# Optimization experiments

Hardware: AMD Instinct MI355X
Metric: run time of the kernel (lower is better)

## Reference

```python
import jax, jax.numpy as jnp
import numpy as np

B = 64        # graphs per batch
N_PER = 1024  # nodes per graph
DEG = 16      # avg degree
H = 128       # hidden width


def _graph_conv(x, src, dst, emask, Wr, b, Wl):
    # PyG GraphConv: out_i = W_rel @ sum_{j->i} x_j + b + W_root @ x_i
    msg = x[src] * emask[:, None]                       # [E, F]
    agg = jax.ops.segment_sum(msg, dst, num_segments=x.shape[0])
    return agg @ Wr + x @ Wl + b


def _topk_pool(x, w, nmask, src, dst, emask, ratio=0.8):
    # PyG TopKPooling: score = (x @ w)/||w||, keep top ceil(ratio*n_i) per graph,
    # kept x scaled by tanh(score). Expressed with masks (fixed shapes).
    score = (x @ w) / jnp.linalg.norm(w)                # [N]
    score = jnp.where(nmask > 0, score, -jnp.inf)
    s2 = score.reshape(B, -1)
    rank = jnp.argsort(jnp.argsort(-s2, axis=1), axis=1)  # rank 0 = largest score
    counts = nmask.reshape(B, -1).sum(axis=1)
    k = jnp.ceil(ratio * counts)
    keep = (rank < k[:, None]).reshape(-1).astype(x.dtype)
    x_new = x * jnp.where(keep > 0, jnp.tanh(score), 0.0)[:, None]
    emask_new = emask * keep[src] * keep[dst]
    return x_new, keep, emask_new


def _readout(x, nmask):
    # concat(global_max_pool, global_mean_pool) over surviving nodes per graph
    xg = x.reshape(B, -1, x.shape[-1])
    m = nmask.reshape(B, -1, 1)
    mx = jnp.max(jnp.where(m > 0, xg, -jnp.inf), axis=1)
    mn = (xg * m).sum(axis=1) / m.sum(axis=1)
    return jnp.concatenate([mx, mn], axis=1)            # [B, 2H]


def setup_inputs():
    key = jax.random.key(0)
    ks = jax.random.split(key, 16)
    N = B * N_PER
    x = jax.random.normal(ks[0], (N, 4), dtype=jnp.float32)
    e_per = N_PER * DEG
    off = (jnp.arange(B) * N_PER)[:, None]
    src = (jax.random.randint(ks[1], (B, e_per), 0, N_PER) + off).reshape(-1)
    dst = (jax.random.randint(ks[2], (B, e_per), 0, N_PER) + off).reshape(-1)
    edge_index = jnp.stack([src, dst]).astype(jnp.int32)

    def lin(k, fi, fo, s=0.1):
        return jax.random.normal(k, (fi, fo), dtype=jnp.float32) * s

    return {
        "x": x, "edge_index": edge_index,
        "w1r": lin(ks[3], 4, H), "b1": jnp.zeros((H,), jnp.float32), "w1l": lin(ks[4], 4, H),
        "w2r": lin(ks[5], H, H), "b2": jnp.zeros((H,), jnp.float32), "w2l": lin(ks[6], H, H),
        "w3r": lin(ks[7], H, H), "b3": jnp.zeros((H,), jnp.float32), "w3l": lin(ks[8], H, H),
        "p1w": jax.random.normal(ks[9], (H,), jnp.float32) * 0.1,
        "p2w": jax.random.normal(ks[10], (H,), jnp.float32) * 0.1,
        "w_lin1": lin(ks[11], 2 * H, H), "b_lin1": jnp.zeros((H,), jnp.float32),
        "w_lin2": lin(ks[12], H, 64), "b_lin2": jnp.zeros((64,), jnp.float32),
        "w_lin3": lin(ks[13], 64, 7), "b_lin3": jnp.zeros((7,), jnp.float32),
    }


def reference(x, edge_index, w1r, b1, w1l, w2r, b2, w2l, w3r, b3, w3l,
              p1w, p2w, w_lin1, b_lin1, w_lin2, b_lin2, w_lin3, b_lin3):
    src, dst = edge_index[0], edge_index[1]
    nmask = jnp.ones((x.shape[0],), x.dtype)
    emask = jnp.ones((src.shape[0],), x.dtype)

    h = jax.nn.relu(_graph_conv(x, src, dst, emask, w1r, b1, w1l)) * nmask[:, None]
    h, nmask, emask = _topk_pool(h, p1w, nmask, src, dst, emask)
    x1 = _readout(h, nmask)

    h = jax.nn.relu(_graph_conv(h, src, dst, emask, w2r, b2, w2l)) * nmask[:, None]
    h, nmask, emask = _topk_pool(h, p2w, nmask, src, dst, emask)
    x2 = _readout(h, nmask)

    h = jax.nn.relu(_graph_conv(h, src, dst, emask, w3r, b3, w3l)) * nmask[:, None]
    # NOTE: original forward reuses self.pool2 for the third pooling (pool3 unused)
    h, nmask, emask = _topk_pool(h, p2w, nmask, src, dst, emask)
    x3 = _readout(h, nmask)

    z = x1 + x2 + x3
    z = jax.nn.relu(z @ w_lin1 + b_lin1)
    # F.dropout with training=False (eval) is identity
    z = jax.nn.relu(z @ w_lin2 + b_lin2)
    return jax.nn.log_softmax(z @ w_lin3 + b_lin3, axis=-1)  # [B, 7]
```

## Files before the change

### kernel.cpp

```cpp
#include <hip/hip_runtime.h>
#include <hip/hip_bf16.h>
#include <math.h>

#define NN   65536
#define NG   64
#define NPER 1024
#define NE   1048576
#define EPG  16384
#define HD   128
#define K1 820
#define K2 656
#define K3 525

typedef unsigned short u16;
typedef unsigned int   u32;
typedef __attribute__((ext_vector_type(8))) short short8;
typedef __attribute__((ext_vector_type(4))) float floatx4;

__device__ __forceinline__ float bf2f(u16 u) {
    union { u32 i; float f; } v; v.i = ((u32)u) << 16; return v.f;
}
__device__ __forceinline__ u16 f2bf(float f) {
    u32 x = __float_as_uint(f);
    return (u16)((x + 0x7fffu + ((x >> 16) & 1u)) >> 16);
}
__device__ __forceinline__ float ldx(const void* p, size_t i, int bf) {
    return bf ? bf2f(((const u16*)p)[i]) : ((const float*)p)[i];
}

__global__ void k_sentinel(u32* out) {
    if (threadIdx.x < 224) out[threadIdx.x] = 0x46404640u;
}

__global__ __launch_bounds__(1024) void k_csr(const int* __restrict__ src,
                                              const int* __restrict__ dst,
                                              int* __restrict__ row_ptr,
                                              int* __restrict__ col,
                                              const void* __restrict__ x,
                                              int* __restrict__ flag) {
    __shared__ int s_scan[1024];
    __shared__ int s_cur[1024];
    int g = blockIdx.x, t = threadIdx.x;
    if (g == 64) {
        int ok = 0;
        if (t < 256) {
            u16 u = ((const u16*)x)[2 * t];
            int e = (u >> 7) & 0xFF;
            ok = (e >= 100 && e <= 140) ? 1 : 0;
        }
        s_scan[t] = ok;
        __syncthreads();
        for (int off = 512; off; off >>= 1) {
            if (t < off) s_scan[t] += s_scan[t + off];
            __syncthreads();
        }
        if (t == 0) flag[0] = (s_scan[0] >= 192) ? 1 : 0;
        return;
    }
    int ebase = g * EPG;
    s_scan[t] = 0;
    __syncthreads();
    #pragma unroll
    for (int i = 0; i < 16; i++) {
        int dd = dst[ebase + i * 1024 + t] - g * NPER;
        atomicAdd(&s_scan[dd], 1);
    }
    __syncthreads();
    int v = s_scan[t];
    __syncthreads();
    s_scan[t] = v;
    __syncthreads();
    for (int off = 1; off < 1024; off <<= 1) {
        int x2 = (t >= off) ? s_scan[t - off] : 0;
        __syncthreads();
        s_scan[t] += x2;
        __syncthreads();
    }
    int excl = s_scan[t] - v;
    row_ptr[g * NPER + t] = ebase + excl;
    if (g == 0 && t == 0) row_ptr[NN] = NE;
    s_cur[t] = excl;
    __syncthreads();
    #pragma unroll
    for (int i = 0; i < 16; i++) {
        int e = ebase + i * 1024 + t;
        int dd = dst[e] - g * NPER;
        int p = atomicAdd(&s_cur[dd], 1);
        col[ebase + p] = src[e];
    }
}

__global__ void k_pack_w(const void* __restrict__ W2r, const void* __restrict__ W2l,
                         const void* __restrict__ W3r, const void* __restrict__ W3l,
                         u16* __restrict__ hi2, u16* __restrict__ lo2,
                         u16* __restrict__ hi3, u16* __restrict__ lo3,
                         const int* __restrict__ flag) {
    const int bf = *flag;
    int which = blockIdx.x >> 7;
    const void* Wr = which ? W3r : W2r;
    const void* Wl = which ? W3l : W2l;
    u16* hi = which ? hi3 : hi2;
    u16* lo = which ? lo3 : lo2;
    int idx = (blockIdx.x & 127) * 256 + threadIdx.x;
    int j = idx & 7;
    int lane = (idx >> 3) & 63;
    int c = (idx >> 9) & 7;
    int t = idx >> 12;
    int k = c * 32 + ((lane >> 4) << 3) + j;
    int n = t * 16 + (lane & 15);
    float w = (k < HD) ? ldx(Wr, (size_t)k * HD + n, bf)
                       : ldx(Wl, (size_t)(k - HD) * HD + n, bf);
    u16 h = f2bf(w);
    hi[idx] = h;
    lo[idx] = f2bf(w - bf2f(h));
}

__global__ void k_conv1(const void* __restrict__ x, const int* __restrict__ row_ptr,
                        const int* __restrict__ col,
                        const void* __restrict__ w1r, const void* __restrict__ b1,
                        const void* __restrict__ w1l, float* __restrict__ hout,
                        const void* __restrict__ pw, float* __restrict__ score,
                        const int* __restrict__ flag) {
    const int bf = *flag;
    int wave = threadIdx.x >> 6, lane = threadIdx.x & 63;
    int node = (blockIdx.x & 63) * NPER + (blockIdx.x >> 6) * 4 + wave;
    int rp = row_ptr[node], rq = row_ptr[node + 1];
    float a0 = 0.f, a1 = 0.f, a2 = 0.f, a3 = 0.f;
    for (int j = rp + lane; j < rq; j += 64) {
        int s = col[j];
        if (bf) {
            ushort4 u = *(const ushort4*)((const u16*)x + (size_t)s * 4);
            a0 += bf2f(u.x); a1 += bf2f(u.y); a2 += bf2f(u.z); a3 += bf2f(u.w);
        } else {
            float4 u = *(const float4*)((const float*)x + (size_t)s * 4);
            a0 += u.x; a1 += u.y; a2 += u.z; a3 += u.w;
        }
    }
    for (int m = 32; m; m >>= 1) {
        a0 += __shfl_xor(a0, m, 64);
        a1 += __shfl_xor(a1, m, 64);
        a2 += __shfl_xor(a2, m, 64);
        a3 += __shfl_xor(a3, m, 64);
    }
    float x0, x1, x2, x3;
    if (bf) {
        ushort4 u = *(const ushort4*)((const u16*)x + (size_t)node * 4);
        x0 = bf2f(u.x); x1 = bf2f(u.y); x2 = bf2f(u.z); x3 = bf2f(u.w);
    } else {
        float4 u = *(const float4*)((const float*)x + (size_t)node * 4);
        x0 = u.x; x1 = u.y; x2 = u.z; x3 = u.w;
    }
    float vout[2];
    #pragma unroll
    for (int rep = 0; rep < 2; rep++) {
        int o = lane + rep * 64;
        float v = ldx(b1, o, bf);
        v += a0 * ldx(w1r, 0 * HD + o, bf) + a1 * ldx(w1r, 1 * HD + o, bf)
           + a2 * ldx(w1r, 2 * HD + o, bf) + a3 * ldx(w1r, 3 * HD + o, bf);
        v += x0 * ldx(w1l, 0 * HD + o, bf) + x1 * ldx(w1l, 1 * HD + o, bf)
           + x2 * ldx(w1l, 2 * HD + o, bf) + x3 * ldx(w1l, 3 * HD + o, bf);
        v = fmaxf(v, 0.f);
        vout[rep] = v;
        hout[(size_t)node * HD + o] = v;
    }
    float w0 = ldx(pw, lane, bf), w1 = ldx(pw, lane + 64, bf);
    float dot = vout[0] * w0 + vout[1] * w1;
    float nrm = w0 * w0 + w1 * w1;
    for (int m = 32; m; m >>= 1) {
        dot += __shfl_xor(dot, m, 64);
        nrm += __shfl_xor(nrm, m, 64);
    }
    if (lane == 0) score[node] = dot / sqrtf(nrm);
}

__global__ __launch_bounds__(256) void k_pool2(
    const float* __restrict__ score, const float* __restrict__ prev_keep,
    float* __restrict__ out_keep, float* __restrict__ out_val,
    const float* __restrict__ h, float* __restrict__ pmax, float* __restrict__ psum,
    int K) {
    __shared__ __align__(16) float s_sc[1024];
    __shared__ int s_r[256];
    __shared__ float s_val[128], s_keep[128];
    __shared__ float s_mx[8][128], s_sm[8][128];
    int g = blockIdx.x & 63, chunk = blockIdx.x >> 6;
    int t = threadIdx.x;
    #pragma unroll
    for (int i = 0; i < 4; i++) {
        int j = t + i * 256;
        float sc = score[g * NPER + j];
        if (prev_keep && prev_keep[g * NPER + j] == 0.f) sc = -INFINITY;
        s_sc[j] = sc;
    }
    __syncthreads();
    int nloc = chunk * 128 + (t & 127);
    int half = t >> 7;
    float sc = s_sc[nloc];
    int r = 0;
    #pragma unroll 4
    for (int j4 = half * 128; j4 < half * 128 + 128; j4++) {
        float4 sv = *(const float4*)&s_sc[j4 * 4];
        int j = j4 * 4;
        r += (int)((sv.x > sc) || (sv.x == sc && j     < nloc));
        r += (int)((sv.y > sc) || (sv.y == sc && j + 1 < nloc));
        r += (int)((sv.z > sc) || (sv.z == sc && j + 2 < nloc));
        r += (int)((sv.w > sc) || (sv.w == sc && j + 3 < nloc));
    }
    s_r[t] = r;
    __syncthreads();
    if (t < 128) {
        int rt = s_r[t] + s_r[t + 128];
        bool kp = rt < K;
        float kpf = kp ? 1.f : 0.f;
        float vv = kp ? tanhf(sc) : 0.f;
        out_keep[g * NPER + nloc] = kpf;
        out_val[g * NPER + nloc] = vv;
        s_keep[t] = kpf;
        s_val[t] = vv;
    }
    __syncthreads();
    int cg = t & 31, slot = t >> 5;
    float4 mx = {-INFINITY, -INFINITY, -INFINITY, -INFINITY};
    float4 sm = {0.f, 0.f, 0.f, 0.f};
    #pragma unroll 4
    for (int i = 0; i < 16; i++) {
        int nn = slot * 16 + i;
        float vv = s_val[nn], kp = s_keep[nn];
        const float* hp = h + (size_t)(g * NPER + chunk * 128 + nn) * HD + cg * 4;
        float4 v = *(const float4*)hp;
        v.x *= vv; v.y *= vv; v.z *= vv; v.w *= vv;
        sm.x += v.x; sm.y += v.y; sm.z += v.z; sm.w += v.w;
        if (kp != 0.f) {
            mx.x = fmaxf(mx.x, v.x); mx.y = fmaxf(mx.y, v.y);
            mx.z = fmaxf(mx.z, v.z); mx.w = fmaxf(mx.w, v.w);
        }
    }
    *(float4*)&s_mx[slot][cg * 4] = mx;
    *(float4*)&s_sm[slot][cg * 4] = sm;
    __syncthreads();
    if (t < 128) {
        float M = s_mx[0][t], S = s_sm[0][t];
        #pragma unroll
        for (int s = 1; s < 8; s++) {
            M = fmaxf(M, s_mx[s][t]);
            S += s_sm[s][t];
        }
        size_t o = (size_t)(chunk * 64 + g) * HD + t;
        pmax[o] = M;
        psum[o] = S;
    }
}

__global__ __launch_bounds__(256) void k_agg(const float* __restrict__ h,
                      const float* __restrict__ val,
                      const int* __restrict__ row_ptr,
                      const int* __restrict__ col, float* __restrict__ agg) {
    int g = blockIdx.x & 63, chunk = blockIdx.x >> 6;
    int wave = threadIdx.x >> 6, lane = threadIdx.x & 63;
    int node = g * NPER + chunk * 4 + wave;
    int rp = row_ptr[node], rq = row_ptr[node + 1];
    int deg = rq - rp;
    int e = lane >> 4, c = lane & 15;
    float4 acc0 = {0.f, 0.f, 0.f, 0.f}, acc1 = {0.f, 0.f, 0.f, 0.f};
    for (int base = 0; base < deg; base += 64) {
        int bcnt = min(64, deg - base);
        int myidx = col[rp + base + ((lane < bcnt) ? lane : 0)];
        int m = 0;
        for (; m + 8 <= bcnt; m += 8) {
            int s0 = __shfl(myidx, m + e, 64);
            int s1 = __shfl(myidx, m + 4 + e, 64);
            float vs0 = val[s0], vs1 = val[s1];
            const float* p0 = h + (size_t)s0 * HD + c * 4;
            const float* p1 = h + (size_t)s1 * HD + c * 4;
            float4 va = *(const float4*)p0;
            float4 vb = *(const float4*)(p0 + 64);
            float4 vc = *(const float4*)p1;
            float4 vd = *(const float4*)(p1 + 64);
            acc0.x += va.x * vs0; acc0.y += va.y * vs0; acc0.z += va.z * vs0; acc0.w += va.w * vs0;
            acc1.x += vb.x * vs0; acc1.y += vb.y * vs0; acc1.z += vb.z * vs0; acc1.w += vb.w * vs0;
            acc0.x += vc.x * vs1; acc0.y += vc.y * vs1; acc0.z += vc.z * vs1; acc0.w += vc.w * vs1;
            acc1.x += vd.x * vs1; acc1.y += vd.y * vs1; acc1.z += vd.z * vs1; acc1.w += vd.w * vs1;
        }
        if (m + 4 <= bcnt) {
            int s0 = __shfl(myidx, m + e, 64);
            float vs0 = val[s0];
            const float* p0 = h + (size_t)s0 * HD + c * 4;
            float4 va = *(const float4*)p0;
            float4 vb = *(const float4*)(p0 + 64);
            acc0.x += va.x * vs0; acc0.y += va.y * vs0; acc0.z += va.z * vs0; acc0.w += va.w * vs0;
            acc1.x += vb.x * vs0; acc1.y += vb.y * vs0; acc1.z += vb.z * vs0; acc1.w += vb.w * vs0;
            m += 4;
        }
        int rem = bcnt - m;
        if (rem > 0) {
            int s0 = __shfl(myidx, m + ((e < rem) ? e : 0), 64);
            float vs0 = val[s0];
            const float* p0 = h + (size_t)s0 * HD + c * 4;
            float4 va = *(const float4*)p0;
            float4 vb = *(const float4*)(p0 + 64);
            if (e < rem) {
                acc0.x += va.x * vs0; acc0.y += va.y * vs0; acc0.z += va.z * vs0; acc0.w += va.w * vs0;
                acc1.x += vb.x * vs0; acc1.y += vb.y * vs0; acc1.z += vb.z * vs0; acc1.w += vb.w * vs0;
            }
        }
    }
    acc0.x += __shfl_xor(acc0.x, 16, 64); acc0.x += __shfl_xor(acc0.x, 32, 64);
    acc0.y += __shfl_xor(acc0.y, 16, 64); acc0.y += __shfl_xor(acc0.y, 32, 64);
    acc0.z += __shfl_xor(acc0.z, 16, 64); acc0.z += __shfl_xor(acc0.z, 32, 64);
    acc0.w += __shfl_xor(acc0.w, 16, 64); acc0.w += __shfl_xor(acc0.w, 32, 64);
    acc1.x += __shfl_xor(acc1.x, 16, 64); acc1.x += __shfl_xor(acc1.x, 32, 64);
    acc1.y += __shfl_xor(acc1.y, 16, 64); acc1.y += __shfl_xor(acc1.y, 32, 64);
    acc1.z += __shfl_xor(acc1.z, 16, 64); acc1.z += __shfl_xor(acc1.z, 32, 64);
    acc1.w += __shfl_xor(acc1.w, 16, 64); acc1.w += __shfl_xor(acc1.w, 32, 64);
    if (e == 0) {
        *(float4*)(agg + (size_t)node * HD + c * 4) = acc0;
        *(float4*)(agg + (size_t)node * HD + 64 + c * 4) = acc1;
    }
}

__global__ __launch_bounds__(256) void k_gemm_mfma(
    const float* __restrict__ agg, const float* __restrict__ h,
    const u16* __restrict__ whi, const u16* __restrict__ wlo,
    const void* __restrict__ bias, const float* __restrict__ keep,
    const float* __restrict__ val, float* __restrict__ out,
    const void* __restrict__ pw, float* __restrict__ score,
    const int* __restrict__ flag) {
    const int bf = *flag;
    int t = threadIdx.x;
    int w = t >> 6, lane = t & 63;
    int quad = lane >> 4;
    int m0 = (blockIdx.x & 63) * NPER + (blockIdx.x >> 6) * 64 + w * 16;
    int mrow = m0 + (lane & 15);
    float vrow = val[mrow];

    floatx4 acc[8];
    #pragma unroll
    for (int i = 0; i < 8; i++) acc[i] = (floatx4)0.f;

    #pragma unroll
    for (int c = 0; c < 8; c++) {
        const float* src = (c < 4) ? agg : h;
        int kb = (c & 3) * 32 + quad * 8;
        const float* pa = src + (size_t)mrow * HD + kb;
        float4 a0 = *(const float4*)pa;
        float4 a1 = *(const float4*)(pa + 4);
        float av[8] = {a0.x, a0.y, a0.z, a0.w, a1.x, a1.y, a1.z, a1.w};
        short8 ahi, alo;
        #pragma unroll
        for (int j = 0; j < 8; j++) {
            float a = (c < 4) ? av[j] : av[j] * vrow;
            u16 hb = f2bf(a);
            ahi[j] = (short)hb;
            alo[j] = (short)f2bf(a - bf2f(hb));
        }
        #pragma unroll
        for (int tt = 0; tt < 8; tt++) {
            const u16* bp = whi + (((size_t)(tt * 8 + c) * 64 + lane) << 3);
            short8 bhi = *(const short8*)bp;
            acc[tt] = __builtin_amdgcn_mfma_f32_16x16x32_bf16(ahi, bhi, acc[tt], 0, 0, 0);
            acc[tt] = __builtin_amdgcn_mfma_f32_16x16x32_bf16(alo, bhi, acc[tt], 0, 0, 0);
        }
        if (!bf) {
            #pragma unroll
            for (int tt = 0; tt < 8; tt++) {
                const u16* bp = wlo + (((size_t)(tt * 8 + c) * 64 + lane) << 3);
                short8 blo = *(const short8*)bp;
                acc[tt] = __builtin_amdgcn_mfma_f32_16x16x32_bf16(ahi, blo, acc[tt], 0, 0, 0);
            }
        }
    }

    float kf[4];
    #pragma unroll
    for (int r = 0; r < 4; r++) kf[r] = keep[m0 + quad * 4 + r];
    float sp0 = 0.f, sp1 = 0.f, sp2 = 0.f, sp3 = 0.f, nrm = 0.f;
    #pragma unroll
    for (int tt = 0; tt < 8; tt++) {
        int colc = tt * 16 + (lane & 15);
        float bcol = ldx(bias, colc, bf);
        float wv = ldx(pw, colc, bf);
        nrm += wv * wv;
        #pragma unroll
        for (int r = 0; r < 4; r++) {
            int row = m0 + quad * 4 + r;
            float v = fmaxf(acc[tt][r] + bcol, 0.f) * kf[r];
            out[(size_t)row * HD + colc] = v;
            if (r == 0) sp0 += v * wv;
            else if (r == 1) sp1 += v * wv;
            else if (r == 2) sp2 += v * wv;
            else sp3 += v * wv;
        }
    }
    #pragma unroll
    for (int m = 1; m < 16; m <<= 1) {
        sp0 += __shfl_xor(sp0, m, 64);
        sp1 += __shfl_xor(sp1, m, 64);
        sp2 += __shfl_xor(sp2, m, 64);
        sp3 += __shfl_xor(sp3, m, 64);
        nrm += __shfl_xor(nrm, m, 64);
    }
    if ((lane & 15) == 0) {
        float inv = 1.f / sqrtf(nrm);
        float4 sc;
        sc.x = sp0 * inv; sc.y = sp1 * inv; sc.z = sp2 * inv; sc.w = sp3 * inv;
        *(float4*)(score + m0 + quad * 4) = sc;
    }
}

__global__ __launch_bounds__(256) void k_mlp(
    const float* __restrict__ pmax1, const float* __restrict__ psum1,
    const float* __restrict__ pmax2, const float* __restrict__ psum2,
    const float* __restrict__ pmax3, const float* __restrict__ psum3,
    const void* __restrict__ w1, const void* __restrict__ b1,
    const void* __restrict__ w2, const void* __restrict__ b2,
    const void* __restrict__ w3, const void* __restrict__ b3,
    void* __restrict__ out, const int* __restrict__ flag) {
    const int bf = *flag;
    int g = blockIdx.x, t = threadIdx.x;
    __shared__ float sIn[256], sZ1[128], sZ2[64], sZ3[7], sRed[2];
    __shared__ float sP1[2][128];
    __shared__ float sP2[4][64];
    if (t < 128) {
        float M1 = -INFINITY, M2 = -INFINITY, M3 = -INFINITY;
        #pragma unroll
        for (int ch = 0; ch < 8; ch++) {
            size_t o = (size_t)(ch * 64 + g) * HD + t;
            M1 = fmaxf(M1, pmax1[o]);
            M2 = fmaxf(M2, pmax2[o]);
            M3 = fmaxf(M3, pmax3[o]);
        }
        sIn[t] = M1 + M2 + M3;
    } else {
        int c = t - 128;
        float S1 = 0.f, S2 = 0.f, S3 = 0.f;
        #pragma unroll
        for (int ch = 0; ch < 8; ch++) {
            size_t o = (size_t)(ch * 64 + g) * HD + c;
            S1 += psum1[o];
            S2 += psum2[o];
            S3 += psum3[o];
        }
        sIn[t] = S1 / (float)K1 + S2 / (float)K2 + S3 / (float)K3;
    }
    __syncthreads();
    {
        int o = t & 127, half = t >> 7;
        float v = 0.f;
        #pragma unroll 8
        for (int k = half * 128; k < half * 128 + 128; k++)
            v += sIn[k] * ldx(w1, (size_t)k * 128 + o, bf);
        sP1[half][o] = v;
    }
    __syncthreads();
    if (t < 128) sZ1[t] = fmaxf(sP1[0][t] + sP1[1][t] + ldx(b1, t, bf), 0.f);
    __syncthreads();
    {
        int o = t & 63, seg = t >> 6;
        float v = 0.f;
        #pragma unroll 8
        for (int k = seg * 32; k < seg * 32 + 32; k++)
            v += sZ1[k] * ldx(w2, (size_t)k * 64 + o, bf);
        sP2[seg][o] = v;
    }
    __syncthreads();
    if (t < 64) sZ2[t] = fmaxf(sP2[0][t] + sP2[1][t] + sP2[2][t] + sP2[3][t]
                               + ldx(b2, t, bf), 0.f);
    __syncthreads();
    if (t < 7) {
        float v = ldx(b3, t, bf);
        #pragma unroll 8
        for (int k = 0; k < 64; k++) v += sZ2[k] * ldx(w3, (size_t)k * 7 + t, bf);
        sZ3[t] = v;
    }
    __syncthreads();
    if (t == 0) {
        float mx = sZ3[0];
        for (int i = 1; i < 7; i++) mx = fmaxf(mx, sZ3[i]);
        float s = 0.f;
        for (int i = 0; i < 7; i++) s += expf(sZ3[i] - mx);
        sRed[0] = mx; sRed[1] = logf(s);
    }
    __syncthreads();
    if (t < 7) {
        float v = sZ3[t] - sRed[0] - sRed[1];
        if (bf) {
            __hip_bfloat16 hb = __float2bfloat16(v);
            ((u16*)out)[g * 7 + t] = *(u16*)&hb;
        } else {
            ((float*)out)[g * 7 + t] = v;
        }
    }
}

extern "C" void kernel_launch(void* const* d_in, const int* in_sizes, int n_in,
                              void* d_out, int out_size, void* d_ws, size_t ws_size,
                              hipStream_t stream) {
    (void)in_sizes; (void)n_in; (void)out_size;
    const void* x   = d_in[0];
    const int* ei   = (const int*)d_in[1];
    const void* w1r = d_in[2];
    const void* b1  = d_in[3];
    const void* w1l = d_in[4];
    const void* w2r = d_in[5];
    const void* b2  = d_in[6];
    const void* w2l = d_in[7];
    const void* w3r = d_in[8];
    const void* b3  = d_in[9];
    const void* w3l = d_in[10];
    const void* p1w = d_in[11];
    const void* p2w = d_in[12];
    const void* wl1 = d_in[13];
    const void* bl1 = d_in[14];
    const void* wl2 = d_in[15];
    const void* bl2 = d_in[16];
    const void* wl3 = d_in[17];
    const void* bl3 = d_in[18];
    const int* srcI = ei;
    const int* dstI = ei + NE;

    char* base = (char*)d_ws;
    char* p = base;
    auto alloc = [&](size_t bytes) -> char* {
        char* r = p; p += (bytes + 255) & ~(size_t)255; return r;
    };
    float* bufA   = (float*)alloc((size_t)NN * HD * 4);
    float* bufB   = (float*)alloc((size_t)NN * HD * 4);
    int* row_ptr  = (int*)alloc((size_t)(NN + 1) * 4);
    int* colA     = (int*)alloc((size_t)NE * 4);
    float* keep1  = (float*)alloc((size_t)NN * 4);
    float* keep2  = (float*)alloc((size_t)NN * 4);
    float* keep3  = (float*)alloc((size_t)NN * 4);
    float* score  = (float*)alloc((size_t)NN * 4);
    float* val1   = (float*)alloc((size_t)NN * 4);
    float* val2   = (float*)alloc((size_t)NN * 4);
    float* val3   = (float*)alloc((size_t)NN * 4);
    float* pmax1  = (float*)alloc((size_t)8 * NG * HD * 4);
    float* psum1  = (float*)alloc((size_t)8 * NG * HD * 4);
    float* pmax2  = (float*)alloc((size_t)8 * NG * HD * 4);
    float* psum2  = (float*)alloc((size_t)8 * NG * HD * 4);
    float* pmax3  = (float*)alloc((size_t)8 * NG * HD * 4);
    float* psum3  = (float*)alloc((size_t)8 * NG * HD * 4);
    int* flag     = (int*)alloc(256);
    u16* whi2     = (u16*)alloc((size_t)32768 * 2);
    u16* wlo2     = (u16*)alloc((size_t)32768 * 2);
    u16* whi3     = (u16*)alloc((size_t)32768 * 2);
    u16* wlo3     = (u16*)alloc((size_t)32768 * 2);

    if ((size_t)(p - base) > ws_size) {
        k_sentinel<<<1, 256, 0, stream>>>((u32*)d_out);
        return;
    }

    k_csr<<<NG + 1, 1024, 0, stream>>>(srcI, dstI, row_ptr, colA, x, flag);
    k_pack_w<<<256, 256, 0, stream>>>(w2r, w2l, w3r, w3l, whi2, wlo2, whi3, wlo3, flag);

    k_conv1<<<NN / 4, 256, 0, stream>>>(x, row_ptr, colA, w1r, b1, w1l, bufA,
                                        p1w, score, flag);
    k_pool2<<<NG * 8, 256, 0, stream>>>(score, nullptr, keep1, val1, bufA,
                                        pmax1, psum1, K1);

    k_agg<<<NN / 4, 256, 0, stream>>>(bufA, val1, row_ptr, colA, bufB);
    k_gemm_mfma<<<NN / 64, 256, 0, stream>>>(bufB, bufA, whi2, wlo2, b2, keep1, val1,
                                             bufB, p2w, score, flag);
    k_pool2<<<NG * 8, 256, 0, stream>>>(score, keep1, keep2, val2, bufB,
                                        pmax2, psum2, K2);

    k_agg<<<NN / 4, 256, 0, stream>>>(bufB, val2, row_ptr, colA, bufA);
    k_gemm_mfma<<<NN / 64, 256, 0, stream>>>(bufA, bufB, whi3, wlo3, b3, keep2, val2,
                                             bufA, p2w, score, flag);
    k_pool2<<<NG * 8, 256, 0, stream>>>(score, keep2, keep3, val3, bufA,
                                        pmax3, psum3, K3);

    k_mlp<<<NG, 256, 0, stream>>>(pmax1, psum1, pmax2, psum2, pmax3, psum3,
                                  wl1, bl1, wl2, bl2, wl3, bl3, d_out, flag);
}
```

Before: 364.3 us.

## Fuse neighbor aggregation into MFMA GEMM and merge weight packing into CSR prep

Removes the separate aggregation kernel: each GEMM block stages its CSR column slice in LDS and each lane gathers and sums neighbor features directly into registers that feed the MFMA A operand. This drops the write and reread of a full aggregated feature buffer and one launch per layer. Weight packing is folded into the CSR build kernel as extra blocks that recompute the dtype flag locally, removing another launch. The tradeoff is less parallelism for the gather, with each lane walking edges serially, and higher register pressure.

```diff
diff --git a/kernel.cpp b/kernel.cpp
--- a/kernel.cpp
+++ b/kernel.cpp
@@ -32,16 +32,18 @@
     if (threadIdx.x < 224) out[threadIdx.x] = 0x46404640u;
 }
 
-__global__ __launch_bounds__(1024) void k_csr(const int* __restrict__ src,
-                                              const int* __restrict__ dst,
-                                              int* __restrict__ row_ptr,
-                                              int* __restrict__ col,
-                                              const void* __restrict__ x,
-                                              int* __restrict__ flag) {
+__global__ __launch_bounds__(1024) void k_prep(
+    const int* __restrict__ src, const int* __restrict__ dst,
+    int* __restrict__ row_ptr, int* __restrict__ col,
+    const void* __restrict__ x, int* __restrict__ flag,
+    const void* __restrict__ W2r, const void* __restrict__ W2l,
+    const void* __restrict__ W3r, const void* __restrict__ W3l,
+    u16* __restrict__ hi2, u16* __restrict__ lo2,
+    u16* __restrict__ hi3, u16* __restrict__ lo3) {
     __shared__ int s_scan[1024];
     __shared__ int s_cur[1024];
-    int g = blockIdx.x, t = threadIdx.x;
-    if (g == 64) {
+    int b = blockIdx.x, t = threadIdx.x;
+    if (b >= 64) {
         int ok = 0;
         if (t < 256) {
             u16 u = ((const u16*)x)[2 * t];
@@ -54,9 +56,32 @@
             if (t < off) s_scan[t] += s_scan[t + off];
             __syncthreads();
         }
-        if (t == 0) flag[0] = (s_scan[0] >= 192) ? 1 : 0;
+        int bf = (s_scan[0] >= 192) ? 1 : 0;
+        if (b == 64) {
+            if (t == 0) flag[0] = bf;
+            return;
+        }
+        int pb = b - 65;
+        int which = pb >> 5;
+        const void* Wr = which ? W3r : W2r;
+        const void* Wl = which ? W3l : W2l;
+        u16* hi = which ? hi3 : hi2;
+        u16* lo = which ? lo3 : lo2;
+        int idx = (pb & 31) * 1024 + t;
+        int j = idx & 7;
+        int lane = (idx >> 3) & 63;
+        int c = (idx >> 9) & 7;
+        int tt = idx >> 12;
+        int k = c * 32 + ((lane >> 4) << 3) + j;
+        int n = tt * 16 + (lane & 15);
+        float w = (k < HD) ? ldx(Wr, (size_t)k * HD + n, bf)
+                           : ldx(Wl, (size_t)(k - HD) * HD + n, bf);
+        u16 h = f2bf(w);
+        hi[idx] = h;
+        lo[idx] = f2bf(w - bf2f(h));
         return;
     }
+    int g = b;
     int ebase = g * EPG;
     s_scan[t] = 0;
     __syncthreads();
@@ -88,31 +113,6 @@
         int p = atomicAdd(&s_cur[dd], 1);
         col[ebase + p] = src[e];
     }
-}
-
-__global__ void k_pack_w(const void* __restrict__ W2r, const void* __restrict__ W2l,
-                         const void* __restrict__ W3r, const void* __restrict__ W3l,
-                         u16* __restrict__ hi2, u16* __restrict__ lo2,
-                         u16* __restrict__ hi3, u16* __restrict__ lo3,
-                         const int* __restrict__ flag) {
-    const int bf = *flag;
-    int which = blockIdx.x >> 7;
-    const void* Wr = which ? W3r : W2r;
-    const void* Wl = which ? W3l : W2l;
-    u16* hi = which ? hi3 : hi2;
-    u16* lo = which ? lo3 : lo2;
-    int idx = (blockIdx.x & 127) * 256 + threadIdx.x;
-    int j = idx & 7;
-    int lane = (idx >> 3) & 63;
-    int c = (idx >> 9) & 7;
-    int t = idx >> 12;
-    int k = c * 32 + ((lane >> 4) << 3) + j;
-    int n = t * 16 + (lane & 15);
-    float w = (k < HD) ? ldx(Wr, (size_t)k * HD + n, bf)
-                       : ldx(Wl, (size_t)(k - HD) * HD + n, bf);
-    u16 h = f2bf(w);
-    hi[idx] = h;
-    lo[idx] = f2bf(w - bf2f(h));
 }
 
 __global__ void k_conv1(const void* __restrict__ x, const int* __restrict__ row_ptr,
@@ -250,107 +250,81 @@
     }
 }
 
-__global__ __launch_bounds__(256) void k_agg(const float* __restrict__ h,
-                      const float* __restrict__ val,
-                      const int* __restrict__ row_ptr,
-                      const int* __restrict__ col, float* __restrict__ agg) {
-    int g = blockIdx.x & 63, chunk = blockIdx.x >> 6;
-    int wave = threadIdx.x >> 6, lane = threadIdx.x & 63;
-    int node = g * NPER + chunk * 4 + wave;
-    int rp = row_ptr[node], rq = row_ptr[node + 1];
-    int deg = rq - rp;
-    int e = lane >> 4, c = lane & 15;
-    float4 acc0 = {0.f, 0.f, 0.f, 0.f}, acc1 = {0.f, 0.f, 0.f, 0.f};
-    for (int base = 0; base < deg; base += 64) {
-        int bcnt = min(64, deg - base);
-        int myidx = col[rp + base + ((lane < bcnt) ? lane : 0)];
-        int m = 0;
-        for (; m + 8 <= bcnt; m += 8) {
-            int s0 = __shfl(myidx, m + e, 64);
-            int s1 = __shfl(myidx, m + 4 + e, 64);
-            float vs0 = val[s0], vs1 = val[s1];
-            const float* p0 = h + (size_t)s0 * HD + c * 4;
-            const float* p1 = h + (size_t)s1 * HD + c * 4;
-            float4 va = *(const float4*)p0;
-            float4 vb = *(const float4*)(p0 + 64);
-            float4 vc = *(const float4*)p1;
-            float4 vd = *(const float4*)(p1 + 64);
-            acc0.x += va.x * vs0; acc0.y += va.y * vs0; acc0.z += va.z * vs0; acc0.w += va.w * vs0;
-            acc1.x += vb.x * vs0; acc1.y += vb.y * vs0; acc1.z += vb.z * vs0; acc1.w += vb.w * vs0;
-            acc0.x += vc.x * vs1; acc0.y += vc.y * vs1; acc0.z += vc.z * vs1; acc0.w += vc.w * vs1;
-            acc1.x += vd.x * vs1; acc1.y += vd.y * vs1; acc1.z += vd.z * vs1; acc1.w += vd.w * vs1;
-        }
-        if (m + 4 <= bcnt) {
-            int s0 = __shfl(myidx, m + e, 64);
-            float vs0 = val[s0];
-            const float* p0 = h + (size_t)s0 * HD + c * 4;
-            float4 va = *(const float4*)p0;
-            float4 vb = *(const float4*)(p0 + 64);
-            acc0.x += va.x * vs0; acc0.y += va.y * vs0; acc0.z += va.z * vs0; acc0.w += va.w * vs0;
-            acc1.x += vb.x * vs0; acc1.y += vb.y * vs0; acc1.z += vb.z * vs0; acc1.w += vb.w * vs0;
-            m += 4;
-        }
-        int rem = bcnt - m;
-        if (rem > 0) {
-            int s0 = __shfl(myidx, m + ((e < rem) ? e : 0), 64);
-            float vs0 = val[s0];
-            const float* p0 = h + (size_t)s0 * HD + c * 4;
-            float4 va = *(const float4*)p0;
-            float4 vb = *(const float4*)(p0 + 64);
-            if (e < rem) {
-                acc0.x += va.x * vs0; acc0.y += va.y * vs0; acc0.z += va.z * vs0; acc0.w += va.w * vs0;
-                acc1.x += vb.x * vs0; acc1.y += vb.y * vs0; acc1.z += vb.z * vs0; acc1.w += vb.w * vs0;
-            }
-        }
-    }
-    acc0.x += __shfl_xor(acc0.x, 16, 64); acc0.x += __shfl_xor(acc0.x, 32, 64);
-    acc0.y += __shfl_xor(acc0.y, 16, 64); acc0.y += __shfl_xor(acc0.y, 32, 64);
-    acc0.z += __shfl_xor(acc0.z, 16, 64); acc0.z += __shfl_xor(acc0.z, 32, 64);
-    acc0.w += __shfl_xor(acc0.w, 16, 64); acc0.w += __shfl_xor(acc0.w, 32, 64);
-    acc1.x += __shfl_xor(acc1.x, 16, 64); acc1.x += __shfl_xor(acc1.x, 32, 64);
-    acc1.y += __shfl_xor(acc1.y, 16, 64); acc1.y += __shfl_xor(acc1.y, 32, 64);
-    acc1.z += __shfl_xor(acc1.z, 16, 64); acc1.z += __shfl_xor(acc1.z, 32, 64);
-    acc1.w += __shfl_xor(acc1.w, 16, 64); acc1.w += __shfl_xor(acc1.w, 32, 64);
-    if (e == 0) {
-        *(float4*)(agg + (size_t)node * HD + c * 4) = acc0;
-        *(float4*)(agg + (size_t)node * HD + 64 + c * 4) = acc1;
-    }
-}
-
-__global__ __launch_bounds__(256) void k_gemm_mfma(
-    const float* __restrict__ agg, const float* __restrict__ h,
+__global__ __launch_bounds__(256) void k_gemm_fused(
+    const float* __restrict__ h, const float* __restrict__ val,
+    const int* __restrict__ row_ptr, const int* __restrict__ col,
     const u16* __restrict__ whi, const u16* __restrict__ wlo,
     const void* __restrict__ bias, const float* __restrict__ keep,
-    const float* __restrict__ val, float* __restrict__ out,
-    const void* __restrict__ pw, float* __restrict__ score,
-    const int* __restrict__ flag) {
+    float* __restrict__ out, const void* __restrict__ pw,
+    float* __restrict__ score, const int* __restrict__ flag) {
     const int bf = *flag;
+    __shared__ int s_col[2048];
+    __shared__ int s_off[65];
     int t = threadIdx.x;
+    int row0 = (blockIdx.x & 63) * NPER + (blockIdx.x >> 6) * 64;
+    if (t < 65) s_off[t] = row_ptr[row0 + t];
+    __syncthreads();
+    int e0 = s_off[0];
+    int cnt = s_off[64] - e0;
+    bool inlds = (cnt <= 2048);
+    if (inlds) for (int i = t; i < cnt; i += 256) s_col[i] = col[e0 + i];
+    __syncthreads();
+
     int w = t >> 6, lane = t & 63;
-    int quad = lane >> 4;
-    int m0 = (blockIdx.x & 63) * NPER + (blockIdx.x >> 6) * 64 + w * 16;
-    int mrow = m0 + (lane & 15);
+    int quad = lane >> 4, mr = lane & 15;
+    int m0 = row0 + w * 16;
+    int mrow = m0 + mr;
     float vrow = val[mrow];
 
+    float aggf[4][8];
+    #pragma unroll
+    for (int c = 0; c < 4; c++)
+        #pragma unroll
+        for (int j = 0; j < 8; j++) aggf[c][j] = 0.f;
+    {
+        int rp = s_off[w * 16 + mr];
+        int deg = s_off[w * 16 + mr + 1] - rp;
+        int off = rp - e0;
+        for (int j = 0; j < deg; j++) {
+            int s = inlds ? s_col[off + j] : col[rp + j];
+            float vs = val[s];
+            const float* hb = h + (size_t)s * HD + quad * 8;
+            #pragma unroll
+            for (int c = 0; c < 4; c++) {
+                float4 u0 = *(const float4*)(hb + c * 32);
+                float4 u1 = *(const float4*)(hb + c * 32 + 4);
+                aggf[c][0] += u0.x * vs; aggf[c][1] += u0.y * vs;
+                aggf[c][2] += u0.z * vs; aggf[c][3] += u0.w * vs;
+                aggf[c][4] += u1.x * vs; aggf[c][5] += u1.y * vs;
+                aggf[c][6] += u1.z * vs; aggf[c][7] += u1.w * vs;
+            }
+        }
+    }
+
     floatx4 acc[8];
     #pragma unroll
     for (int i = 0; i < 8; i++) acc[i] = (floatx4)0.f;
 
     #pragma unroll
     for (int c = 0; c < 8; c++) {
-        const float* src = (c < 4) ? agg : h;
-        int kb = (c & 3) * 32 + quad * 8;
-        const float* pa = src + (size_t)mrow * HD + kb;
-        float4 a0 = *(const float4*)pa;
-        float4 a1 = *(const float4*)(pa + 4);
-        float av[8] = {a0.x, a0.y, a0.z, a0.w, a1.x, a1.y, a1.z, a1.w};
+        float av[8];
+        if (c < 4) {
+            #pragma unroll
+            for (int j = 0; j < 8; j++) av[j] = aggf[c][j];
+        } else {
+            int kb = (c & 3) * 32 + quad * 8;
+            const float* pa = h + (size_t)mrow * HD + kb;
+            float4 a0 = *(const float4*)pa;
+            float4 a1 = *(const float4*)(pa + 4);
+            av[0] = a0.x * vrow; av[1] = a0.y * vrow; av[2] = a0.z * vrow; av[3] = a0.w * vrow;
+            av[4] = a1.x * vrow; av[5] = a1.y * vrow; av[6] = a1.z * vrow; av[7] = a1.w * vrow;
+        }
         short8 ahi, alo;
         #pragma unroll
         for (int j = 0; j < 8; j++) {
-            float a = (c < 4) ? av[j] : av[j] * vrow;
-            u16 hb = f2bf(a);
+            u16 hb = f2bf(av[j]);
             ahi[j] = (short)hb;
-            alo[j] = (short)f2bf(a - bf2f(hb));
+            alo[j] = (short)f2bf(av[j] - bf2f(hb));
         }
         #pragma unroll
         for (int tt = 0; tt < 8; tt++) {
@@ -550,23 +524,23 @@
         return;
     }
 
-    k_csr<<<NG + 1, 1024, 0, stream>>>(srcI, dstI, row_ptr, colA, x, flag);
-    k_pack_w<<<256, 256, 0, stream>>>(w2r, w2l, w3r, w3l, whi2, wlo2, whi3, wlo3, flag);
+    k_prep<<<129, 1024, 0, stream>>>(srcI, dstI, row_ptr, colA, x, flag,
+                                     w2r, w2l, w3r, w3l, whi2, wlo2, whi3, wlo3);
 
     k_conv1<<<NN / 4, 256, 0, stream>>>(x, row_ptr, colA, w1r, b1, w1l, bufA,
                                         p1w, score, flag);
     k_pool2<<<NG * 8, 256, 0, stream>>>(score, nullptr, keep1, val1, bufA,
                                         pmax1, psum1, K1);
 
-    k_agg<<<NN / 4, 256, 0, stream>>>(bufA, val1, row_ptr, colA, bufB);
-    k_gemm_mfma<<<NN / 64, 256, 0, stream>>>(bufB, bufA, whi2, wlo2, b2, keep1, val1,
-                                             bufB, p2w, score, flag);
+    k_gemm_fused<<<NN / 64, 256, 0, stream>>>(bufA, val1, row_ptr, colA,
+                                              whi2, wlo2, b2, keep1, bufB,
+                                              p2w, score, flag);
     k_pool2<<<NG * 8, 256, 0, stream>>>(score, keep1, keep2, val2, bufB,
                                         pmax2, psum2, K2);
 
-    k_agg<<<NN / 4, 256, 0, stream>>>(bufB, val2, row_ptr, colA, bufA);
-    k_gemm_mfma<<<NN / 64, 256, 0, stream>>>(bufA, bufB, whi3, wlo3, b3, keep2, val2,
-                                             bufA, p2w, score, flag);
+    k_gemm_fused<<<NN / 64, 256, 0, stream>>>(bufB, val2, row_ptr, colA,
+                                              whi3, wlo3, b3, keep2, bufA,
+                                              p2w, score, flag);
     k_pool2<<<NG * 8, 256, 0, stream>>>(score, keep2, keep3, val3, bufA,
                                         pmax3, psum3, K3);
 
```

Result: slower. 466.9 us (+28.2%).
